# Performance work log

Measured on AMD Instinct MI355X. Metric: run time of the kernel, lower is better.

The kernel has to match this reference:

```python
import jax, jax.numpy as jnp
import numpy as np

N, E, D, H = 50000, 500000, 128, 8
DH = D // H  # per-head dim = int(out_dim // num_heads)
EPS_LN = 1e-5
EPS_BN = 1e-5


def _ln(x, g, b):
    m = x.mean(-1, keepdims=True)
    v = ((x - m) ** 2).mean(-1, keepdims=True)
    return (x - m) * jax.lax.rsqrt(v + EPS_LN) * g + b


def _bn(x, g, b):
    # BatchNorm1d, training-mode statistics (biased variance over the batch)
    m = x.mean(0)
    v = ((x - m) ** 2).mean(0)
    return (x - m) * jax.lax.rsqrt(v + EPS_BN) * g + b


def setup_inputs() -> dict:
    key = jax.random.key(0)
    ks = jax.random.split(key, 16)
    rn = lambda k, shape: (jax.random.normal(k, shape, jnp.float32) * 0.05)
    h = jax.random.normal(ks[0], (N, D), jnp.float32)
    src = jax.random.randint(ks[1], (E,), 0, N).astype(jnp.int32)
    # guarantee every node receives at least one message so z > 0 (no 0/0)
    dst = jnp.concatenate([jnp.arange(N, dtype=jnp.int32),
                           jax.random.randint(ks[2], (E - N,), 0, N).astype(jnp.int32)])
    return {
        "h": h, "src": src, "dst": dst,
        # per-node TransformerEncoder (seq_len == 1 subgraphs)
        "Win": rn(ks[3], (3 * D, D)), "bin": jnp.zeros((3 * D,), jnp.float32),
        "Wout": rn(ks[4], (D, D)), "bout": jnp.zeros((D,), jnp.float32),
        "Wte1": rn(ks[5], (4 * D, D)), "bte1": jnp.zeros((4 * D,), jnp.float32),
        "Wte2": rn(ks[6], (D, 4 * D)), "bte2": jnp.zeros((D,), jnp.float32),
        "ln1g": jnp.ones((D,), jnp.float32), "ln1b": jnp.zeros((D,), jnp.float32),
        "ln2g": jnp.ones((D,), jnp.float32), "ln2b": jnp.zeros((D,), jnp.float32),
        # graph multi-head attention projections (use_bias=False)
        "WQ": rn(ks[7], (D, D)), "WK": rn(ks[8], (D, D)), "WV": rn(ks[9], (D, D)),
        # node-wise FFN + batch norms
        "W1": rn(ks[10], (2 * D, D)), "b1": jnp.zeros((2 * D,), jnp.float32),
        "W2": rn(ks[11], (D, 2 * D)), "b2": jnp.zeros((D,), jnp.float32),
        "bn1g": jnp.ones((D,), jnp.float32), "bn1b": jnp.zeros((D,), jnp.float32),
        "bn2g": jnp.ones((D,), jnp.float32), "bn2b": jnp.zeros((D,), jnp.float32),
    }


def _forward(h, src, dst, Win, bin_, Wout, bout, Wte1, bte1, Wte2, bte2,
             ln1g, ln1b, ln2g, ln2b, WQ, WK, WV,
             W1, b1, W2, b2, bn1g, bn1b, bn2g, bn2b):
    # --- per-node TransformerEncoder. Each dgl.node_subgraph(g, [i]) contains
    # only the center node, so self-attention runs over a length-1 sequence:
    # softmax of a single score is 1, hence attn_out = out_proj(v).
    v = h @ Win[2 * D:].T + bin_[2 * D:]            # V slice of in_proj
    x = _ln(h + (v @ Wout.T + bout), ln1g, ln1b)
    ff = jax.nn.relu(x @ Wte1.T + bte1) @ Wte2.T + bte2
    hsub = _ln(x + ff, ln2g, ln2b)                  # [N, D]

    # --- graph multi-head attention (DGL apply_edges / send_and_recv)
    Qh = (hsub @ WQ.T).reshape(N, H, DH)
    Kh = (hsub @ WK.T).reshape(N, H, DH)
    Vh = (hsub @ WV.T).reshape(N, H, DH)
    score = (Kh[src] * Qh[dst]).sum(-1)             # [E, H]  K_src . Q_dst
    score = jnp.exp(jnp.clip(score / np.sqrt(DH), -5.0, 5.0))
    wV = jax.ops.segment_sum(Vh[src] * score[:, :, None], dst, num_segments=N)
    z = jax.ops.segment_sum(score, dst, num_segments=N)
    attn = (wV / z[:, :, None]).reshape(N, D)

    # --- residual + BN + FFN + residual + BN (dropout p=0 / eval mode)
    hh = _bn(hsub + attn, bn1g, bn1b)
    h_in2 = hh
    hh = jax.nn.relu(hh @ W1.T + b1) @ W2.T + b2
    return _bn(h_in2 + hh, bn2g, bn2b)


def reference(h, src, dst, Win, bin, Wout, bout, Wte1, bte1, Wte2, bte2,
              ln1g, ln1b, ln2g, ln2b, WQ, WK, WV,
              W1, b1, W2, b2, bn1g, bn1b, bn2g, bn2b):
    return _forward(h, src, dst, Win, bin, Wout, bout, Wte1, bte1, Wte2, bte2,
                    ln1g, ln1b, ln2g, ln2b, WQ, WK, WV,
                    W1, b1, W2, b2, bn1g, bn1b, bn2g, bn2b)
```

## Files before the change

kernel.cpp:

```cpp
#include <hip/hip_runtime.h>
#include <hip/hip_bf16.h>


#define D_ 128

typedef __attribute__((ext_vector_type(8))) short short8;
typedef __attribute__((ext_vector_type(4))) short short4v;
typedef __attribute__((ext_vector_type(4))) float f32x4;

__device__ __forceinline__ float b2f(ushort u) {
    union { uint u32; float f; } x; x.u32 = ((uint)u) << 16; return x.f;
}
__device__ __forceinline__ ushort f2b(float f) {
    union { __hip_bfloat16 h; ushort u; } v; v.h = __float2bfloat16(f); return v.u;
}

template<int AMODE, int EPI, bool RELU, bool RESF32>
__global__ __launch_bounds__(512) void gemm_bf16(
    const void* __restrict__ Aptr, const ushort* __restrict__ W,
    const float* __restrict__ bias, void* __restrict__ C,
    const float* __restrict__ bn_in, float* __restrict__ bn_out,
    const float* __restrict__ bng, const float* __restrict__ bnb,
    const void* __restrict__ resid, const ushort* __restrict__ y1res,
    const float* __restrict__ lng, const float* __restrict__ lnb,
    float invn, int n, int K, int M)
{
    __shared__ ushort Abuf[128 * 32];
    __shared__ ushort Bbuf[128 * 32];
    __shared__ float s_sh[128], t_sh[128];

    const int t    = threadIdx.x;
    const int lane = t & 63;
    const int w    = t >> 6;
    const int r0   = blockIdx.x * 128;
    const int c0   = blockIdx.y * 128;
    const int wr   = (w >> 1) * 32;
    const int wc   = (w & 1) * 64;
    const int rl   = lane & 15;
    const int kh   = lane >> 4;

    if (AMODE == 2 || EPI == 2) {
        if (t < 128) {
            float m   = bn_in[t] * invn;
            float var = bn_in[128 + t] * invn - m * m;
            float rs  = rsqrtf(var + 1e-5f);
            float s   = rs * bng[t];
            s_sh[t] = s;
            t_sh[t] = bnb[t] - m * s;
        }
        __syncthreads();
    }

    f32x4 acc[2][4] = {};

    for (int kc = 0; kc < K; kc += 32) {
        const int row = t >> 2, pos = t & 3;
        if (AMODE == 1) {
            const int ch = pos;
            int gr = r0 + row;
            short8 aval = {};
            if (gr < n) {
                const float* Af = (const float*)Aptr;
                float4 f0 = *reinterpret_cast<const float4*>(Af + (size_t)gr * K + kc + ch * 8);
                float4 f1 = *reinterpret_cast<const float4*>(Af + (size_t)gr * K + kc + ch * 8 + 4);
                aval[0] = (short)f2b(f0.x); aval[1] = (short)f2b(f0.y);
                aval[2] = (short)f2b(f0.z); aval[3] = (short)f2b(f0.w);
                aval[4] = (short)f2b(f1.x); aval[5] = (short)f2b(f1.y);
                aval[6] = (short)f2b(f1.z); aval[7] = (short)f2b(f1.w);
            }
            short8 bval = *reinterpret_cast<const short8*>(W + (size_t)(c0 + row) * K + kc + ch * 8);
            __syncthreads();
            int sw = ch ^ ((row >> 1) & 3);
            *reinterpret_cast<short8*>(&Abuf[row * 32 + sw * 8]) = aval;
            *reinterpret_cast<short8*>(&Bbuf[row * 32 + sw * 8]) = bval;
            __syncthreads();
        } else {
            __syncthreads();
            const int ch = pos ^ ((row >> 1) & 3);
            const ushort* srcA = (const ushort*)Aptr + (size_t)(r0 + row) * K + kc + ch * 8;
            const ushort* srcB = W + (size_t)(c0 + row) * K + kc + ch * 8;
            __builtin_amdgcn_global_load_lds(
                (const __attribute__((address_space(1))) void*)srcA,
                (__attribute__((address_space(3))) void*)&Abuf[t * 8], 16, 0, 0);
            __builtin_amdgcn_global_load_lds(
                (const __attribute__((address_space(1))) void*)srcB,
                (__attribute__((address_space(3))) void*)&Bbuf[t * 8], 16, 0, 0);
            __syncthreads();
        }

        short8 af[2], bfr[4];
        #pragma unroll
        for (int m = 0; m < 2; ++m) {
            int rr = wr + m * 16 + rl;
            af[m] = *reinterpret_cast<const short8*>(&Abuf[rr * 32 + (kh ^ ((rr >> 1) & 3)) * 8]);
        }
        if (AMODE == 2) {
            #pragma unroll
            for (int m = 0; m < 2; ++m) {
                short8 v = af[m];
                #pragma unroll
                for (int q = 0; q < 8; ++q) {
                    int cch = kc + kh * 8 + q;
                    v[q] = (short)f2b(fmaf(b2f((ushort)v[q]), s_sh[cch], t_sh[cch]));
                }
                af[m] = v;
            }
        }
        #pragma unroll
        for (int nn = 0; nn < 4; ++nn) {
            int col = wc + nn * 16 + rl;
            bfr[nn] = *reinterpret_cast<const short8*>(&Bbuf[col * 32 + (kh ^ ((col >> 1) & 3)) * 8]);
        }
        #pragma unroll
        for (int m = 0; m < 2; ++m)
            #pragma unroll
            for (int nn = 0; nn < 4; ++nn)
                acc[m][nn] = __builtin_amdgcn_mfma_f32_16x16x32_bf16(
                    bfr[nn], af[m], acc[m][nn], 0, 0, 0);
    }

    const int ch4 = kh * 4;

    if (EPI == 1) {
        __shared__ float lnS[128][2], lnS2[128][2];
        float4 bb[4];
        #pragma unroll
        for (int nn = 0; nn < 4; ++nn)
            bb[nn] = *reinterpret_cast<const float4*>(bias + wc + nn * 16 + ch4);
        #pragma unroll
        for (int m = 0; m < 2; ++m) {
            int r = r0 + wr + m * 16 + rl;
            float s = 0.f, s2 = 0.f;
            #pragma unroll
            for (int nn = 0; nn < 4; ++nn) {
                int c = wc + nn * 16 + ch4;
                float rv[4] = {0.f, 0.f, 0.f, 0.f};
                if (r < n) {
                    if (RESF32) {
                        float4 f = *reinterpret_cast<const float4*>((const float*)resid + (size_t)r * 128 + c);
                        rv[0] = f.x; rv[1] = f.y; rv[2] = f.z; rv[3] = f.w;
                    } else {
                        short4v f = *reinterpret_cast<const short4v*>((const ushort*)resid + (size_t)r * 128 + c);
                        rv[0] = b2f((ushort)f[0]); rv[1] = b2f((ushort)f[1]);
                        rv[2] = b2f((ushort)f[2]); rv[3] = b2f((ushort)f[3]);
                    }
                }
                float bj[4] = {bb[nn].x, bb[nn].y, bb[nn].z, bb[nn].w};
                #pragma unroll
                for (int j = 0; j < 4; ++j) {
                    float o = acc[m][nn][j] + bj[j] + rv[j];
                    acc[m][nn][j] = o;
                    s += o; s2 += o * o;
                }
            }
            s  += __shfl_xor(s, 16);  s  += __shfl_xor(s, 32);
            s2 += __shfl_xor(s2, 16); s2 += __shfl_xor(s2, 32);
            if (kh == 0) {
                lnS[wr + m * 16 + rl][w & 1]  = s;
                lnS2[wr + m * 16 + rl][w & 1] = s2;
            }
        }
        __syncthreads();
        #pragma unroll
        for (int m = 0; m < 2; ++m) {
            int rloc = wr + m * 16 + rl;
            int r = r0 + rloc;
            float S  = lnS[rloc][0] + lnS[rloc][1];
            float S2 = lnS2[rloc][0] + lnS2[rloc][1];
            float mean = S * (1.f / 128.f);
            float var  = S2 * (1.f / 128.f) - mean * mean;
            float rs   = rsqrtf(var + 1e-5f);
            if (r >= n) continue;
            #pragma unroll
            for (int nn = 0; nn < 4; ++nn) {
                int c = wc + nn * 16 + ch4;
                float4 gv = *reinterpret_cast<const float4*>(lng + c);
                float4 bv = *reinterpret_cast<const float4*>(lnb + c);
                float gj[4] = {gv.x, gv.y, gv.z, gv.w};
                float bj[4] = {bv.x, bv.y, bv.z, bv.w};
                short4v p;
                #pragma unroll
                for (int j = 0; j < 4; ++j)
                    p[j] = (short)f2b((acc[m][nn][j] - mean) * rs * gj[j] + bj[j]);
                *reinterpret_cast<short4v*>((ushort*)C + (size_t)r * 128 + c) = p;
            }
        }
        return;
    }

    if (EPI == 2) {
        __shared__ float csum[128], csum2[128];
        if (t < 128) { csum[t] = 0.f; csum2[t] = 0.f; }
        __syncthreads();
        float ps[4][4] = {};
        float ps2[4][4] = {};
        #pragma unroll
        for (int m = 0; m < 2; ++m) {
            int r = r0 + wr + m * 16 + rl;
            bool ok = r < n;
            #pragma unroll
            for (int nn = 0; nn < 4; ++nn) {
                int c = wc + nn * 16 + ch4;
                float4 bb = *reinterpret_cast<const float4*>(bias + c);
                float bj[4] = {bb.x, bb.y, bb.z, bb.w};
                short4v yv = {};
                if (ok) yv = *reinterpret_cast<const short4v*>(y1res + (size_t)r * 128 + c);
                short4v p;
                #pragma unroll
                for (int j = 0; j < 4; ++j) {
                    float o = 0.f;
                    if (ok) {
                        o = acc[m][nn][j] + bj[j]
                          + fmaf(b2f((ushort)yv[j]), s_sh[c + j], t_sh[c + j]);
                    }
                    ps[nn][j] += o; ps2[nn][j] += o * o;
                    p[j] = (short)f2b(o);
                }
                if (ok)
                    *reinterpret_cast<short4v*>((ushort*)C + (size_t)r * 128 + c) = p;
            }
        }
        #pragma unroll
        for (int nn = 0; nn < 4; ++nn)
            #pragma unroll
            for (int j = 0; j < 4; ++j) {
                float a = ps[nn][j], b = ps2[nn][j];
                #pragma unroll
                for (int o2 = 1; o2 < 16; o2 <<= 1) {
                    a += __shfl_xor(a, o2);
                    b += __shfl_xor(b, o2);
                }
                if (rl == 0) {
                    int c = wc + nn * 16 + ch4 + j;
                    atomicAdd(&csum[c], a);
                    atomicAdd(&csum2[c], b);
                }
            }
        __syncthreads();
        if (t < 128) {
            atomicAdd(bn_out + t, csum[t]);
            atomicAdd(bn_out + 128 + t, csum2[t]);
        }
        return;
    }

    #pragma unroll
    for (int m = 0; m < 2; ++m) {
        int r = r0 + wr + m * 16 + rl;
        if (r >= n) continue;
        #pragma unroll
        for (int nn = 0; nn < 4; ++nn) {
            int c = c0 + wc + nn * 16 + ch4;
            f32x4 vacc = acc[m][nn];
            float4 bb = make_float4(0.f, 0.f, 0.f, 0.f);
            if (bias) bb = *reinterpret_cast<const float4*>(bias + c);
            float o0 = vacc[0] + bb.x, o1 = vacc[1] + bb.y;
            float o2 = vacc[2] + bb.z, o3 = vacc[3] + bb.w;
            if (RELU) {
                o0 = fmaxf(o0, 0.f); o1 = fmaxf(o1, 0.f);
                o2 = fmaxf(o2, 0.f); o3 = fmaxf(o3, 0.f);
            }
            short4v p;
            p[0] = (short)f2b(o0); p[1] = (short)f2b(o1);
            p[2] = (short)f2b(o2); p[3] = (short)f2b(o3);
            *reinterpret_cast<short4v*>((ushort*)C + (size_t)r * M + c) = p;
        }
    }
}

__global__ void hist_kernel(const int* __restrict__ dst, int* __restrict__ cnt, int E_)
{
    int e = blockIdx.x * blockDim.x + threadIdx.x;
    if (e < E_) atomicAdd(cnt + dst[e], 1);
}

__global__ __launch_bounds__(256) void scan_block_kernel(
    int* __restrict__ data, int* __restrict__ bsum, int n)
{
    __shared__ int tmp[256];
    int i = blockIdx.x * 256 + threadIdx.x;
    int v = (i < n) ? data[i] : 0;
    tmp[threadIdx.x] = v;
    __syncthreads();
    #pragma unroll
    for (int o = 1; o < 256; o <<= 1) {
        int y = (threadIdx.x >= o) ? tmp[threadIdx.x - o] : 0;
        __syncthreads();
        tmp[threadIdx.x] += y;
        __syncthreads();
    }
    if (i < n) data[i] = tmp[threadIdx.x] - v;
    if (threadIdx.x == 255) bsum[blockIdx.x] = tmp[255];
}

__global__ __launch_bounds__(256) void scan_bsum_kernel(int* __restrict__ bsum, int nb)
{
    __shared__ int tmp[256];
    int v = (threadIdx.x < nb) ? bsum[threadIdx.x] : 0;
    tmp[threadIdx.x] = v;
    __syncthreads();
    #pragma unroll
    for (int o = 1; o < 256; o <<= 1) {
        int y = (threadIdx.x >= o) ? tmp[threadIdx.x - o] : 0;
        __syncthreads();
        tmp[threadIdx.x] += y;
        __syncthreads();
    }
    if (threadIdx.x < nb) bsum[threadIdx.x] = tmp[threadIdx.x] - v;
}

__global__ void add_off_kernel(int* __restrict__ data, const int* __restrict__ bsum, int n)
{
    int i = blockIdx.x * blockDim.x + threadIdx.x;
    if (i < n) data[i] += bsum[i >> 8];
}

__global__ void scatter_kernel(const int* __restrict__ src, const int* __restrict__ dst,
                               int* __restrict__ rowptr, int* __restrict__ csr_src, int E_)
{
    int e = blockIdx.x * blockDim.x + threadIdx.x;
    if (e >= E_) return;
    int pos = atomicAdd(rowptr + dst[e], 1);
    csr_src[pos] = src[e];
}

__global__ __launch_bounds__(256) void attn_agg_kernel(
    const int* __restrict__ rowptr, const int* __restrict__ csr_src,
    const ushort* __restrict__ QKV, const ushort* __restrict__ hsub,
    ushort* __restrict__ out, int n)
{
    int node = (blockIdx.x * blockDim.x + threadIdx.x) >> 6;
    if (node >= n) return;
    int lane = threadIdx.x & 63;
    int slot = lane >> 3;
    int hd   = lane & 7;
    int start = node ? rowptr[node - 1] : 0;
    int end   = rowptr[node];

    const ushort* qp = QKV + (size_t)node * 384 + hd * 16;
    short8 q0 = *reinterpret_cast<const short8*>(qp);
    short8 q1 = *reinterpret_cast<const short8*>(qp + 8);
    float q[16];
    #pragma unroll
    for (int i = 0; i < 8; ++i) { q[i] = b2f((ushort)q0[i]); q[8 + i] = b2f((ushort)q1[i]); }

    float acc[16] = {};
    float zh = 0.f;
    for (int j = start; j < end; j += 8) {
        int idx  = j + slot;
        bool act = idx < end;
        int s = csr_src[act ? idx : start];
        const ushort* kp = QKV + (size_t)s * 384 + 128 + hd * 16;
        short8 k0 = *reinterpret_cast<const short8*>(kp);
        short8 k1 = *reinterpret_cast<const short8*>(kp + 8);
        float p = 0.f;
        #pragma unroll
        for (int i = 0; i < 8; ++i) {
            p = fmaf(b2f((ushort)k0[i]), q[i], p);
            p = fmaf(b2f((ushort)k1[i]), q[8 + i], p);
        }
        float sc = act ? __expf(fminf(fmaxf(p * 0.25f, -5.f), 5.f)) : 0.f;
        short8 v0 = *reinterpret_cast<const short8*>(kp + 128);
        short8 v1 = *reinterpret_cast<const short8*>(kp + 136);
        #pragma unroll
        for (int i = 0; i < 8; ++i) {
            acc[i]     = fmaf(sc, b2f((ushort)v0[i]), acc[i]);
            acc[8 + i] = fmaf(sc, b2f((ushort)v1[i]), acc[8 + i]);
        }
        zh += sc;
    }
    #pragma unroll
    for (int i = 0; i < 16; ++i) {
        acc[i] += __shfl_xor(acc[i], 8);
        acc[i] += __shfl_xor(acc[i], 16);
        acc[i] += __shfl_xor(acc[i], 32);
    }
    zh += __shfl_xor(zh, 8);
    zh += __shfl_xor(zh, 16);
    zh += __shfl_xor(zh, 32);

    if (slot == 0) {
        const ushort* hp = hsub + (size_t)node * D_ + hd * 16;
        short8 h0 = *reinterpret_cast<const short8*>(hp);
        short8 h1 = *reinterpret_cast<const short8*>(hp + 8);
        float inv = 1.f / zh;
        short8 o0, o1;
        #pragma unroll
        for (int i = 0; i < 8; ++i) {
            o0[i] = (short)f2b(b2f((ushort)h0[i]) + acc[i] * inv);
            o1[i] = (short)f2b(b2f((ushort)h1[i]) + acc[8 + i] * inv);
        }
        ushort* op = out + (size_t)node * D_ + hd * 16;
        *reinterpret_cast<short8*>(op)     = o0;
        *reinterpret_cast<short8*>(op + 8) = o1;
    }
}

__global__ __launch_bounds__(256) void bn_stats_kernel(
    const ushort* __restrict__ x, float* __restrict__ sums, int n)
{
    int c    = threadIdx.x & 127;
    int half = threadIdx.x >> 7;
    float s = 0.f, s2 = 0.f;
    for (int r = blockIdx.x * 2 + half; r < n; r += gridDim.x * 2) {
        float v = b2f(x[(size_t)r * D_ + c]);
        s += v; s2 += v * v;
    }
    __shared__ float ls[256], ls2[256];
    ls[threadIdx.x] = s; ls2[threadIdx.x] = s2;
    __syncthreads();
    if (half == 0) {
        s  += ls[threadIdx.x + 128];
        s2 += ls2[threadIdx.x + 128];
        atomicAdd(sums + c, s);
        atomicAdd(sums + 128 + c, s2);
    }
}

__global__ void bn_norm_kernel(const ushort* __restrict__ x,
                               const float* __restrict__ stats,
                               const float* __restrict__ g, const float* __restrict__ b,
                               float* __restrict__ out, float invn, int total4)
{
    int i = blockIdx.x * blockDim.x + threadIdx.x;
    if (i >= total4) return;
    int cb = (i << 2) & 127;
    short4v v = reinterpret_cast<const short4v*>(x)[i];
    float4 o;
    float r[4];
    #pragma unroll
    for (int q = 0; q < 4; ++q) {
        int c = cb + q;
        float m   = stats[c] * invn;
        float var = stats[128 + c] * invn - m * m;
        float rs  = rsqrtf(var + 1e-5f);
        r[q] = (b2f((ushort)v[q]) - m) * rs * g[c] + b[c];
    }
    o.x = r[0]; o.y = r[1]; o.z = r[2]; o.w = r[3];
    reinterpret_cast<float4*>(out)[i] = o;
}

__global__ __launch_bounds__(256) void fuse_w_kernel(
    const float* __restrict__ Win, const float* __restrict__ bin_,
    const float* __restrict__ Wout, const float* __restrict__ bout,
    ushort* __restrict__ Wf, float* __restrict__ bf)
{
    int idx = blockIdx.x * 256 + threadIdx.x;
    int i = idx >> 7, c = idx & 127;
    const float* WinV = Win + 256 * 128;
    float s = 0.f;
    for (int j = 0; j < 128; ++j)
        s = fmaf(Wout[i * 128 + j], WinV[j * 128 + c], s);
    Wf[idx] = f2b(s);
    if (c == 0) {
        float tb = bout[i];
        for (int j = 0; j < 128; ++j)
            tb = fmaf(Wout[i * 128 + j], bin_[256 + j], tb);
        bf[i] = tb;
    }
}

struct WPtrs { const float* p[7]; };

__global__ __launch_bounds__(256) void cvt_w_kernel(WPtrs wp, ushort* __restrict__ out)
{
    const int off[8] = {0, 65536, 131072, 147456, 163840, 180224, 212992, 245760};
    int e0 = (blockIdx.x * 256 + threadIdx.x) * 4;
    if (e0 >= 245760) return;
    int s = 0;
    #pragma unroll
    for (int j = 1; j < 7; ++j) if (e0 >= off[j]) s = j;
    float4 f = *reinterpret_cast<const float4*>(wp.p[s] + (e0 - off[s]));
    short4v o;
    o[0] = (short)f2b(f.x); o[1] = (short)f2b(f.y);
    o[2] = (short)f2b(f.z); o[3] = (short)f2b(f.w);
    *reinterpret_cast<short4v*>(out + e0) = o;
}

extern "C" void kernel_launch(void* const* d_in, const int* in_sizes, int n_in,
                              void* d_out, int out_size, void* d_ws, size_t ws_size,
                              hipStream_t stream)
{
    const float* h    = (const float*)d_in[0];
    const int*   src  = (const int*)d_in[1];
    const int*   dst  = (const int*)d_in[2];
    const float* Win  = (const float*)d_in[3];
    const float* bin_ = (const float*)d_in[4];
    const float* Wout = (const float*)d_in[5];
    const float* bout = (const float*)d_in[6];
    const float* Wte1 = (const float*)d_in[7];
    const float* bte1 = (const float*)d_in[8];
    const float* Wte2 = (const float*)d_in[9];
    const float* bte2 = (const float*)d_in[10];
    const float* ln1g = (const float*)d_in[11];
    const float* ln1b = (const float*)d_in[12];
    const float* ln2g = (const float*)d_in[13];
    const float* ln2b = (const float*)d_in[14];
    const float* WQ   = (const float*)d_in[15];
    const float* WK   = (const float*)d_in[16];
    const float* WV   = (const float*)d_in[17];
    const float* W1   = (const float*)d_in[18];
    const float* b1   = (const float*)d_in[19];
    const float* W2   = (const float*)d_in[20];
    const float* b2   = (const float*)d_in[21];
    const float* bn1g = (const float*)d_in[22];
    const float* bn1b = (const float*)d_in[23];
    const float* bn2g = (const float*)d_in[24];
    const float* bn2b = (const float*)d_in[25];

    const int N_ = in_sizes[0] / D_;
    const int E_ = in_sizes[1];
    const size_t S2 = (size_t)N_ * D_ / 2;

    float* ws = (float*)d_ws;
    size_t off_tail = 7 * S2;
    size_t need = (off_tail + 131072 + 128 + 512) * sizeof(float)
                + (size_t)(N_ + E_ + 256) * sizeof(int) + 4096;
    if (ws_size < need) return;

    ushort* bufA   = (ushort*)ws;
    ushort* bufB   = (ushort*)(ws + S2);
    ushort* bufC   = (ushort*)(ws + 2 * S2);
    ushort* bufD   = (ushort*)(ws + 3 * S2);
    ushort* wbf    = (ushort*)(ws + off_tail);
    float*  bfused = ws + off_tail + 131072;
    float*  stats  = bfused + 128;
    int* rowptr  = (int*)(stats + 512);
    int* csr_src = rowptr + N_;
    int* bsum    = csr_src + E_;

    const ushort* Wte1_bf = wbf;
    const ushort* Wte2_bf = wbf + 65536;
    const ushort* WQKV_bf = wbf + 131072;
    const ushort* W1_bf   = wbf + 180224;
    const ushort* W2_bf   = wbf + 212992;
    ushort*       Wf_bf   = wbf + 245760;

    dim3 blk(256);
    dim3 blk512(512);
    const int rowBlocks = (N_ + 127) / 128;
    const int totElems  = N_ * D_;
    const dim3 gRow((N_ + 3) / 4);
    const int nb = (N_ + 255) / 256;
    const float invn = 1.f / (float)N_;

    hipMemsetAsync(stats, 0, 512 * sizeof(float), stream);
    hipMemsetAsync(rowptr, 0, (size_t)N_ * sizeof(int), stream);

    hist_kernel<<<dim3((E_ + 255) / 256), blk, 0, stream>>>(dst, rowptr, E_);
    scan_block_kernel<<<dim3(nb), blk, 0, stream>>>(rowptr, bsum, N_);
    scan_bsum_kernel<<<dim3(1), blk, 0, stream>>>(bsum, nb);
    add_off_kernel<<<dim3(nb), blk, 0, stream>>>(rowptr, bsum, N_);
    scatter_kernel<<<dim3((E_ + 255) / 256), blk, 0, stream>>>(src, dst, rowptr, csr_src, E_);

    fuse_w_kernel<<<dim3(64), blk, 0, stream>>>(Win, bin_, Wout, bout, Wf_bf, bfused);
    WPtrs wp;
    wp.p[0] = Wte1; wp.p[1] = Wte2; wp.p[2] = WQ; wp.p[3] = WK; wp.p[4] = WV;
    wp.p[5] = W1;   wp.p[6] = W2;
    cvt_w_kernel<<<dim3(240), blk, 0, stream>>>(wp, wbf);

    gemm_bf16<1, 1, false, true><<<dim3(rowBlocks, 1), blk512, 0, stream>>>(
        h, Wf_bf, bfused, bufA, nullptr, nullptr, nullptr, nullptr,
        h, nullptr, ln1g, ln1b, 0.f, N_, 128, 128);
    gemm_bf16<0, 0, true, false><<<dim3(rowBlocks, 4), blk512, 0, stream>>>(
        bufA, Wte1_bf, bte1, bufD, nullptr, nullptr, nullptr, nullptr,
        nullptr, nullptr, nullptr, nullptr, 0.f, N_, 128, 512);
    gemm_bf16<0, 1, false, false><<<dim3(rowBlocks, 1), blk512, 0, stream>>>(
        bufD, Wte2_bf, bte2, bufC, nullptr, nullptr, nullptr, nullptr,
        bufA, nullptr, ln2g, ln2b, 0.f, N_, 512, 128);

    gemm_bf16<0, 0, false, false><<<dim3(rowBlocks, 3), blk512, 0, stream>>>(
        bufC, WQKV_bf, nullptr, bufD, nullptr, nullptr, nullptr, nullptr,
        nullptr, nullptr, nullptr, nullptr, 0.f, N_, 128, 384);
    attn_agg_kernel<<<gRow, blk, 0, stream>>>(
        rowptr, csr_src, bufD, bufC, bufA, N_);

    bn_stats_kernel<<<dim3(512), blk, 0, stream>>>(bufA, stats, N_);

    gemm_bf16<2, 0, true, false><<<dim3(rowBlocks, 2), blk512, 0, stream>>>(
        bufA, W1_bf, b1, bufD, stats, nullptr, bn1g, bn1b,
        nullptr, nullptr, nullptr, nullptr, invn, N_, 128, 256);
    gemm_bf16<0, 2, false, false><<<dim3(rowBlocks, 1), blk512, 0, stream>>>(
        bufD, W2_bf, b2, bufB, stats, stats + 256, bn1g, bn1b,
        nullptr, bufA, nullptr, nullptr, invn, N_, 256, 128);
    bn_norm_kernel<<<dim3((totElems / 4 + 255) / 256), blk, 0, stream>>>(
        bufB, stats + 256, bn2g, bn2b, (float*)d_out, invn, totElems / 4);
}
```

Before: 282.9 us.

## Double-buffer GEMM LDS loads, halve attention wave per node, merge prep kernels

The bf16 GEMM now double-buffers its LDS tiles, so the global_load_lds for the next K chunk is issued before the MFMAs on the current chunk, and it needs one barrier per chunk instead of two. Attention aggregation gives each node 32 lanes instead of 64, with 4 edge slots per iteration and a per-slot branch, so each wave covers more nodes. The separate bsum scan kernel is dropped: each add_off block reduces its own prefix of the block sums. The two weight-preparation kernels are merged into one launch and the two memsets into one. These changes cut launch count and hide load latency, at the cost of doubled LDS per GEMM block, which may lower occupancy.

```diff
diff --git a/kernel.cpp b/kernel.cpp
--- a/kernel.cpp
+++ b/kernel.cpp
@@ -25,8 +25,8 @@
     const float* __restrict__ lng, const float* __restrict__ lnb,
     float invn, int n, int K, int M)
 {
-    __shared__ ushort Abuf[128 * 32];
-    __shared__ ushort Bbuf[128 * 32];
+    __shared__ ushort Abuf[2][128 * 32];
+    __shared__ ushort Bbuf[2][128 * 32];
     __shared__ float s_sh[128], t_sh[128];
 
     const int t    = threadIdx.x;
@@ -52,10 +52,12 @@
     }
 
     f32x4 acc[2][4] = {};
-
-    for (int kc = 0; kc < K; kc += 32) {
-        const int row = t >> 2, pos = t & 3;
-        if (AMODE == 1) {
+    const int nc = K >> 5;
+    const int row = t >> 2, pos = t & 3;
+
+    if (AMODE == 1) {
+        for (int c = 0; c < nc; ++c) {
+            int kc = c * 32;
             const int ch = pos;
             int gr = r0 + row;
             short8 aval = {};
@@ -71,52 +73,81 @@
             short8 bval = *reinterpret_cast<const short8*>(W + (size_t)(c0 + row) * K + kc + ch * 8);
             __syncthreads();
             int sw = ch ^ ((row >> 1) & 3);
-            *reinterpret_cast<short8*>(&Abuf[row * 32 + sw * 8]) = aval;
-            *reinterpret_cast<short8*>(&Bbuf[row * 32 + sw * 8]) = bval;
+            *reinterpret_cast<short8*>(&Abuf[0][row * 32 + sw * 8]) = aval;
+            *reinterpret_cast<short8*>(&Bbuf[0][row * 32 + sw * 8]) = bval;
             __syncthreads();
-        } else {
+            short8 af[2], bfr[4];
+            #pragma unroll
+            for (int m = 0; m < 2; ++m) {
+                int rr = wr + m * 16 + rl;
+                af[m] = *reinterpret_cast<const short8*>(&Abuf[0][rr * 32 + (kh ^ ((rr >> 1) & 3)) * 8]);
+            }
+            #pragma unroll
+            for (int nn = 0; nn < 4; ++nn) {
+                int col = wc + nn * 16 + rl;
+                bfr[nn] = *reinterpret_cast<const short8*>(&Bbuf[0][col * 32 + (kh ^ ((col >> 1) & 3)) * 8]);
+            }
+            #pragma unroll
+            for (int m = 0; m < 2; ++m)
+                #pragma unroll
+                for (int nn = 0; nn < 4; ++nn)
+                    acc[m][nn] = __builtin_amdgcn_mfma_f32_16x16x32_bf16(
+                        bfr[nn], af[m], acc[m][nn], 0, 0, 0);
+        }
+    } else {
+        const int ch = pos ^ ((row >> 1) & 3);
+        const ushort* Abase = (const ushort*)Aptr + (size_t)(r0 + row) * K + ch * 8;
+        const ushort* Bbase = W + (size_t)(c0 + row) * K + ch * 8;
+        __builtin_amdgcn_global_load_lds(
+            (const __attribute__((address_space(1))) void*)Abase,
+            (__attribute__((address_space(3))) void*)&Abuf[0][t * 8], 16, 0, 0);
+        __builtin_amdgcn_global_load_lds(
+            (const __attribute__((address_space(1))) void*)Bbase,
+            (__attribute__((address_space(3))) void*)&Bbuf[0][t * 8], 16, 0, 0);
+        __syncthreads();
+        for (int c = 0; c < nc; ++c) {
+            if (c + 1 < nc) {
+                int half = (c + 1) & 1;
+                __builtin_amdgcn_global_load_lds(
+                    (const __attribute__((address_space(1))) void*)(Abase + (c + 1) * 32),
+                    (__attribute__((address_space(3))) void*)&Abuf[half][t * 8], 16, 0, 0);
+                __builtin_amdgcn_global_load_lds(
+                    (const __attribute__((address_space(1))) void*)(Bbase + (c + 1) * 32),
+                    (__attribute__((address_space(3))) void*)&Bbuf[half][t * 8], 16, 0, 0);
+            }
+            const int cur = c & 1;
+            const int kc  = c * 32;
+            short8 af[2], bfr[4];
+            #pragma unroll
+            for (int m = 0; m < 2; ++m) {
+                int rr = wr + m * 16 + rl;
+                af[m] = *reinterpret_cast<const short8*>(&Abuf[cur][rr * 32 + (kh ^ ((rr >> 1) & 3)) * 8]);
+            }
+            if (AMODE == 2) {
+                #pragma unroll
+                for (int m = 0; m < 2; ++m) {
+                    short8 v = af[m];
+                    #pragma unroll
+                    for (int q = 0; q < 8; ++q) {
+                        int cch = kc + kh * 8 + q;
+                        v[q] = (short)f2b(fmaf(b2f((ushort)v[q]), s_sh[cch], t_sh[cch]));
+                    }
+                    af[m] = v;
+                }
+            }
+            #pragma unroll
+            for (int nn = 0; nn < 4; ++nn) {
+                int col = wc + nn * 16 + rl;
+                bfr[nn] = *reinterpret_cast<const short8*>(&Bbuf[cur][col * 32 + (kh ^ ((col >> 1) & 3)) * 8]);
+            }
+            #pragma unroll
+            for (int m = 0; m < 2; ++m)
+                #pragma unroll
+                for (int nn = 0; nn < 4; ++nn)
+                    acc[m][nn] = __builtin_amdgcn_mfma_f32_16x16x32_bf16(
+                        bfr[nn], af[m], acc[m][nn], 0, 0, 0);
             __syncthreads();
-            const int ch = pos ^ ((row >> 1) & 3);
-            const ushort* srcA = (const ushort*)Aptr + (size_t)(r0 + row) * K + kc + ch * 8;
-            const ushort* srcB = W + (size_t)(c0 + row) * K + kc + ch * 8;
-            __builtin_amdgcn_global_load_lds(
-                (const __attribute__((address_space(1))) void*)srcA,
-                (__attribute__((address_space(3))) void*)&Abuf[t * 8], 16, 0, 0);
-            __builtin_amdgcn_global_load_lds(
-                (const __attribute__((address_space(1))) void*)srcB,
-                (__attribute__((address_space(3))) void*)&Bbuf[t * 8], 16, 0, 0);
-            __syncthreads();
-        }
-
-        short8 af[2], bfr[4];
-        #pragma unroll
-        for (int m = 0; m < 2; ++m) {
-            int rr = wr + m * 16 + rl;
-            af[m] = *reinterpret_cast<const short8*>(&Abuf[rr * 32 + (kh ^ ((rr >> 1) & 3)) * 8]);
-        }
-        if (AMODE == 2) {
-            #pragma unroll
-            for (int m = 0; m < 2; ++m) {
-                short8 v = af[m];
-                #pragma unroll
-                for (int q = 0; q < 8; ++q) {
-                    int cch = kc + kh * 8 + q;
-                    v[q] = (short)f2b(fmaf(b2f((ushort)v[q]), s_sh[cch], t_sh[cch]));
-                }
-                af[m] = v;
-            }
-        }
-        #pragma unroll
-        for (int nn = 0; nn < 4; ++nn) {
-            int col = wc + nn * 16 + rl;
-            bfr[nn] = *reinterpret_cast<const short8*>(&Bbuf[col * 32 + (kh ^ ((col >> 1) & 3)) * 8]);
-        }
-        #pragma unroll
-        for (int m = 0; m < 2; ++m)
-            #pragma unroll
-            for (int nn = 0; nn < 4; ++nn)
-                acc[m][nn] = __builtin_amdgcn_mfma_f32_16x16x32_bf16(
-                    bfr[nn], af[m], acc[m][nn], 0, 0, 0);
+        }
     }
 
     const int ch4 = kh * 4;
@@ -293,26 +324,19 @@
     if (threadIdx.x == 255) bsum[blockIdx.x] = tmp[255];
 }
 
-__global__ __launch_bounds__(256) void scan_bsum_kernel(int* __restrict__ bsum, int nb)
-{
-    __shared__ int tmp[256];
-    int v = (threadIdx.x < nb) ? bsum[threadIdx.x] : 0;
-    tmp[threadIdx.x] = v;
+__global__ __launch_bounds__(256) void add_off_kernel(
+    int* __restrict__ data, const int* __restrict__ bsum, int n, int nb)
+{
+    __shared__ int red[4];
+    int b = blockIdx.x;
+    int v = (threadIdx.x < b && threadIdx.x < nb) ? bsum[threadIdx.x] : 0;
+    #pragma unroll
+    for (int o = 1; o < 64; o <<= 1) v += __shfl_xor(v, o);
+    if ((threadIdx.x & 63) == 0) red[threadIdx.x >> 6] = v;
     __syncthreads();
-    #pragma unroll
-    for (int o = 1; o < 256; o <<= 1) {
-        int y = (threadIdx.x >= o) ? tmp[threadIdx.x - o] : 0;
-        __syncthreads();
-        tmp[threadIdx.x] += y;
-        __syncthreads();
-    }
-    if (threadIdx.x < nb) bsum[threadIdx.x] = tmp[threadIdx.x] - v;
-}
-
-__global__ void add_off_kernel(int* __restrict__ data, const int* __restrict__ bsum, int n)
-{
-    int i = blockIdx.x * blockDim.x + threadIdx.x;
-    if (i < n) data[i] += bsum[i >> 8];
+    int off = red[0] + red[1] + red[2] + red[3];
+    int i = b * 256 + threadIdx.x;
+    if (i < n) data[i] += off;
 }
 
 __global__ void scatter_kernel(const int* __restrict__ src, const int* __restrict__ dst,
@@ -329,15 +353,16 @@
     const ushort* __restrict__ QKV, const ushort* __restrict__ hsub,
     ushort* __restrict__ out, int n)
 {
-    int node = (blockIdx.x * blockDim.x + threadIdx.x) >> 6;
-    if (node >= n) return;
-    int lane = threadIdx.x & 63;
-    int slot = lane >> 3;
-    int hd   = lane & 7;
-    int start = node ? rowptr[node - 1] : 0;
-    int end   = rowptr[node];
-
-    const ushort* qp = QKV + (size_t)node * 384 + hd * 16;
+    int node  = (blockIdx.x * blockDim.x + threadIdx.x) >> 5;
+    int lane5 = threadIdx.x & 31;
+    int slot  = lane5 >> 3;
+    int hd    = lane5 & 7;
+    bool valid = node < n;
+    int nd = valid ? node : 0;
+    int start = (valid && nd) ? rowptr[nd - 1] : 0;
+    int end   = valid ? rowptr[nd] : 0;
+
+    const ushort* qp = QKV + (size_t)nd * 384 + hd * 16;
     short8 q0 = *reinterpret_cast<const short8*>(qp);
     short8 q1 = *reinterpret_cast<const short8*>(qp + 8);
     float q[16];
@@ -346,41 +371,40 @@
 
     float acc[16] = {};
     float zh = 0.f;
-    for (int j = start; j < end; j += 8) {
-        int idx  = j + slot;
-        bool act = idx < end;
-        int s = csr_src[act ? idx : start];
-        const ushort* kp = QKV + (size_t)s * 384 + 128 + hd * 16;
-        short8 k0 = *reinterpret_cast<const short8*>(kp);
-        short8 k1 = *reinterpret_cast<const short8*>(kp + 8);
-        float p = 0.f;
-        #pragma unroll
-        for (int i = 0; i < 8; ++i) {
-            p = fmaf(b2f((ushort)k0[i]), q[i], p);
-            p = fmaf(b2f((ushort)k1[i]), q[8 + i], p);
-        }
-        float sc = act ? __expf(fminf(fmaxf(p * 0.25f, -5.f), 5.f)) : 0.f;
-        short8 v0 = *reinterpret_cast<const short8*>(kp + 128);
-        short8 v1 = *reinterpret_cast<const short8*>(kp + 136);
-        #pragma unroll
-        for (int i = 0; i < 8; ++i) {
-            acc[i]     = fmaf(sc, b2f((ushort)v0[i]), acc[i]);
-            acc[8 + i] = fmaf(sc, b2f((ushort)v1[i]), acc[8 + i]);
-        }
-        zh += sc;
+    for (int j = start; j < end; j += 4) {
+        int idx = j + slot;
+        if (idx < end) {
+            int s = csr_src[idx];
+            const ushort* kp = QKV + (size_t)s * 384 + 128 + hd * 16;
+            short8 k0 = *reinterpret_cast<const short8*>(kp);
+            short8 k1 = *reinterpret_cast<const short8*>(kp + 8);
+            float p = 0.f;
+            #pragma unroll
+            for (int i = 0; i < 8; ++i) {
+                p = fmaf(b2f((ushort)k0[i]), q[i], p);
+                p = fmaf(b2f((ushort)k1[i]), q[8 + i], p);
+            }
+            float sc = __expf(fminf(fmaxf(p * 0.25f, -5.f), 5.f));
+            short8 v0 = *reinterpret_cast<const short8*>(kp + 128);
+            short8 v1 = *reinterpret_cast<const short8*>(kp + 136);
+            #pragma unroll
+            for (int i = 0; i < 8; ++i) {
+                acc[i]     = fmaf(sc, b2f((ushort)v0[i]), acc[i]);
+                acc[8 + i] = fmaf(sc, b2f((ushort)v1[i]), acc[8 + i]);
+            }
+            zh += sc;
+        }
     }
     #pragma unroll
     for (int i = 0; i < 16; ++i) {
         acc[i] += __shfl_xor(acc[i], 8);
         acc[i] += __shfl_xor(acc[i], 16);
-        acc[i] += __shfl_xor(acc[i], 32);
     }
     zh += __shfl_xor(zh, 8);
     zh += __shfl_xor(zh, 16);
-    zh += __shfl_xor(zh, 32);
-
-    if (slot == 0) {
-        const ushort* hp = hsub + (size_t)node * D_ + hd * 16;
+
+    if (slot == 0 && valid) {
+        const ushort* hp = hsub + (size_t)nd * D_ + hd * 16;
         short8 h0 = *reinterpret_cast<const short8*>(hp);
         short8 h1 = *reinterpret_cast<const short8*>(hp + 8);
         float inv = 1.f / zh;
@@ -390,7 +414,7 @@
             o0[i] = (short)f2b(b2f((ushort)h0[i]) + acc[i] * inv);
             o1[i] = (short)f2b(b2f((ushort)h1[i]) + acc[8 + i] * inv);
         }
-        ushort* op = out + (size_t)node * D_ + hd * 16;
+        ushort* op = out + (size_t)nd * D_ + hd * 16;
         *reinterpret_cast<short8*>(op)     = o0;
         *reinterpret_cast<short8*>(op + 8) = o1;
     }
@@ -440,41 +464,41 @@
     reinterpret_cast<float4*>(out)[i] = o;
 }
 
-__global__ __launch_bounds__(256) void fuse_w_kernel(
+struct WPtrs { const float* p[7]; };
+
+__global__ __launch_bounds__(256) void prep_w_kernel(
     const float* __restrict__ Win, const float* __restrict__ bin_,
     const float* __restrict__ Wout, const float* __restrict__ bout,
-    ushort* __restrict__ Wf, float* __restrict__ bf)
-{
-    int idx = blockIdx.x * 256 + threadIdx.x;
-    int i = idx >> 7, c = idx & 127;
-    const float* WinV = Win + 256 * 128;
-    float s = 0.f;
-    for (int j = 0; j < 128; ++j)
-        s = fmaf(Wout[i * 128 + j], WinV[j * 128 + c], s);
-    Wf[idx] = f2b(s);
-    if (c == 0) {
-        float tb = bout[i];
+    WPtrs wp, ushort* __restrict__ wbf, float* __restrict__ bfused)
+{
+    int b = blockIdx.x;
+    if (b < 64) {
+        int idx = b * 256 + threadIdx.x;
+        int i = idx >> 7, c = idx & 127;
+        const float* WinV = Win + 256 * 128;
+        float s = 0.f;
         for (int j = 0; j < 128; ++j)
-            tb = fmaf(Wout[i * 128 + j], bin_[256 + j], tb);
-        bf[i] = tb;
-    }
-}
-
-struct WPtrs { const float* p[7]; };
-
-__global__ __launch_bounds__(256) void cvt_w_kernel(WPtrs wp, ushort* __restrict__ out)
-{
-    const int off[8] = {0, 65536, 131072, 147456, 163840, 180224, 212992, 245760};
-    int e0 = (blockIdx.x * 256 + threadIdx.x) * 4;
-    if (e0 >= 245760) return;
-    int s = 0;
-    #pragma unroll
-    for (int j = 1; j < 7; ++j) if (e0 >= off[j]) s = j;
-    float4 f = *reinterpret_cast<const float4*>(wp.p[s] + (e0 - off[s]));
-    short4v o;
-    o[0] = (short)f2b(f.x); o[1] = (short)f2b(f.y);
-    o[2] = (short)f2b(f.z); o[3] = (short)f2b(f.w);
-    *reinterpret_cast<short4v*>(out + e0) = o;
+            s = fmaf(Wout[i * 128 + j], WinV[j * 128 + c], s);
+        wbf[245760 + idx] = f2b(s);
+        if (c == 0) {
+            float tb = bout[i];
+            for (int j = 0; j < 128; ++j)
+                tb = fmaf(Wout[i * 128 + j], bin_[256 + j], tb);
+            bfused[i] = tb;
+        }
+    } else {
+        const int off[8] = {0, 65536, 131072, 147456, 163840, 180224, 212992, 245760};
+        int e0 = ((b - 64) * 256 + threadIdx.x) * 4;
+        if (e0 >= 245760) return;
+        int s = 0;
+        #pragma unroll
+        for (int j = 1; j < 7; ++j) if (e0 >= off[j]) s = j;
+        float4 f = *reinterpret_cast<const float4*>(wp.p[s] + (e0 - off[s]));
+        short4v o;
+        o[0] = (short)f2b(f.x); o[1] = (short)f2b(f.y);
+        o[2] = (short)f2b(f.z); o[3] = (short)f2b(f.w);
+        *reinterpret_cast<short4v*>(wbf + e0) = o;
+    }
 }
 
 extern "C" void kernel_launch(void* const* d_in, const int* in_sizes, int n_in,
@@ -540,24 +564,21 @@
     dim3 blk512(512);
     const int rowBlocks = (N_ + 127) / 128;
     const int totElems  = N_ * D_;
-    const dim3 gRow((N_ + 3) / 4);
+    const dim3 gNode((N_ + 7) / 8);
     const int nb = (N_ + 255) / 256;
     const float invn = 1.f / (float)N_;
 
-    hipMemsetAsync(stats, 0, 512 * sizeof(float), stream);
-    hipMemsetAsync(rowptr, 0, (size_t)N_ * sizeof(int), stream);
+    hipMemsetAsync(stats, 0, (512 + (size_t)N_) * sizeof(float), stream);
 
     hist_kernel<<<dim3((E_ + 255) / 256), blk, 0, stream>>>(dst, rowptr, E_);
     scan_block_kernel<<<dim3(nb), blk, 0, stream>>>(rowptr, bsum, N_);
-    scan_bsum_kernel<<<dim3(1), blk, 0, stream>>>(bsum, nb);
-    add_off_kernel<<<dim3(nb), blk, 0, stream>>>(rowptr, bsum, N_);
+    add_off_kernel<<<dim3(nb), blk, 0, stream>>>(rowptr, bsum, N_, nb);
     scatter_kernel<<<dim3((E_ + 255) / 256), blk, 0, stream>>>(src, dst, rowptr, csr_src, E_);
 
-    fuse_w_kernel<<<dim3(64), blk, 0, stream>>>(Win, bin_, Wout, bout, Wf_bf, bfused);
     WPtrs wp;
     wp.p[0] = Wte1; wp.p[1] = Wte2; wp.p[2] = WQ; wp.p[3] = WK; wp.p[4] = WV;
     wp.p[5] = W1;   wp.p[6] = W2;
-    cvt_w_kernel<<<dim3(240), blk, 0, stream>>>(wp, wbf);
+    prep_w_kernel<<<dim3(304), blk, 0, stream>>>(Win, bin_, Wout, bout, wp, wbf, bfused);
 
     gemm_bf16<1, 1, false, true><<<dim3(rowBlocks, 1), blk512, 0, stream>>>(
         h, Wf_bf, bfused, bufA, nullptr, nullptr, nullptr, nullptr,
@@ -572,7 +593,7 @@
     gemm_bf16<0, 0, false, false><<<dim3(rowBlocks, 3), blk512, 0, stream>>>(
         bufC, WQKV_bf, nullptr, bufD, nullptr, nullptr, nullptr, nullptr,
         nullptr, nullptr, nullptr, nullptr, 0.f, N_, 128, 384);
-    attn_agg_kernel<<<gRow, blk, 0, stream>>>(
+    attn_agg_kernel<<<gNode, blk, 0, stream>>>(
         rowptr, csr_src, bufD, bufC, bufA, N_);
 
     bn_stats_kernel<<<dim3(512), blk, 0, stream>>>(bufA, stats, N_);
```

New measurement: 276.1 us. 2.4% less time.
